# Kernel optimization log

Measured on AMD Instinct MI355X. Metric: run time of the kernel, lower is better.

Reference implementation:

```python
import jax, jax.numpy as jnp
import numpy as np

INPUT_DIM = 4
HIDDEN_DIM = 256
T_OBS, T_UNOBS, BATCH = 64, 32, 4096


def setup_inputs() -> dict:
    key = jax.random.key(0)
    ks = jax.random.split(key, 16)
    H, D = HIDDEN_DIM, INPUT_DIM
    s = lambda k, shape, fan: jax.random.normal(k, shape, jnp.float32) * (1.0 / np.sqrt(fan))
    return {
        "x_obs": jax.random.normal(ks[0], (T_OBS, BATCH, D), jnp.float32),
        "t_obs": jnp.cumsum(jax.random.uniform(ks[1], (T_OBS, BATCH, 1), jnp.float32), axis=0),
        "t_unobs": jax.random.uniform(ks[2], (T_UNOBS, BATCH, 1), jnp.float32),
        # stem MLP (n_layers=2): Linear(D+1 -> H), LeakyReLU, Linear(H -> H)
        "stem_w1": s(ks[3], (H, D + 1), D + 1),
        "stem_b1": jnp.zeros((H,), jnp.float32),
        "stem_w2": s(ks[4], (H, H), H),
        "stem_b2": jnp.zeros((H,), jnp.float32),
        # single-layer GRU, PyTorch gate order (r, z, n)
        "gru_wi": s(ks[5], (3 * H, H), H),
        "gru_wh": s(ks[6], (3 * H, H), H),
        "gru_bi": jnp.zeros((3 * H,), jnp.float32),
        "gru_bh": jnp.zeros((3 * H,), jnp.float32),
        # head MLP (n_layers=1): Linear(H -> D)
        "head_w": s(ks[7], (D, H), H),
        "head_b": jnp.zeros((D,), jnp.float32),
    }


def _gru_cell(x, h, wi, wh, bi, bh):
    # x, h: [B, H].  PyTorch GRU: r,z gates sigmoid; n gate tanh with r gating hidden path.
    gx = x @ wi.T + bi
    gh = h @ wh.T + bh
    rx, zx, nx = jnp.split(gx, 3, axis=-1)
    rh, zh, nh = jnp.split(gh, 3, axis=-1)
    r = jax.nn.sigmoid(rx + rh)
    u = jax.nn.sigmoid(zx + zh)
    n = jnp.tanh(nx + r * nh)
    return (1.0 - u) * n + u * h


def reference(x_obs, t_obs, t_unobs, stem_w1, stem_b1, stem_w2, stem_b2,
              gru_wi, gru_wh, gru_bi, gru_bh, head_w, head_b):
    unobs_len = t_unobs.shape[0]
    batch, hidden = x_obs.shape[1], gru_wh.shape[1]

    # preprocess: first difference of time (0 at step 0), concat, stem MLP
    t_diff = jnp.concatenate([jnp.zeros_like(t_obs[:1]), t_obs[1:] - t_obs[:-1]], axis=0)
    xt = jnp.concatenate([x_obs, t_diff], axis=-1)             # [T_obs, B, D+1]
    xt = jax.nn.leaky_relu(xt @ stem_w1.T + stem_b1)
    xt = xt @ stem_w2.T + stem_b2                              # [T_obs, B, H]

    cell = lambda x, h: _gru_cell(x, jax.lax.stop_gradient(h), gru_wi, gru_wh, gru_bi, gru_bh)

    h0 = jnp.zeros((batch, hidden), x_obs.dtype)

    def obs_step(h, x_t):
        h_new = cell(x_t, h)
        return h_new, None

    h, _ = jax.lax.scan(obs_step, h0, xt)
    z_last = h                                                  # output of 1-layer GRU == hidden

    def ar_step(carry, _):
        z, h = carry
        h_new = cell(z, h)
        return (h_new, h_new), h_new

    (_, _), zs_rest = jax.lax.scan(ar_step, (z_last, h), None, length=unobs_len - 1)
    zs = jnp.concatenate([z_last[None], zs_rest], axis=0)       # [T_unobs, B, H]

    x_hats = zs @ head_w.T + head_b                             # [T_unobs, B, D]
    return x_hats, zs
```

## Files before the change

kernel.cpp:

```cpp
#include <hip/hip_runtime.h>
#include <cstdint>
#include <cstddef>

#define T_OBS_C 64
#define T_UNOBS_C 32
#define BATCH_C 4096
#define HID_C 256

typedef short v8s __attribute__((ext_vector_type(8)));
typedef float v4f __attribute__((ext_vector_type(4)));
typedef unsigned short u16x8 __attribute__((ext_vector_type(8)));

__device__ __forceinline__ float bf2f(unsigned short u) {
  union { unsigned int i; float f; } v; v.i = ((unsigned int)u) << 16; return v.f;
}
__device__ __forceinline__ unsigned short f2bf(float f) {
  union { float f; unsigned int i; } v; v.f = f;
  unsigned int r = (v.i + 0x7FFFu + ((v.i >> 16) & 1u)) >> 16;
  return (unsigned short)r;
}

__global__ void prep_kernel(const float* __restrict__ wi,
                            const float* __restrict__ w2,
                            const float* __restrict__ b2,
                            const float* __restrict__ bi,
                            unsigned short* __restrict__ wi_hi,
                            unsigned short* __restrict__ wi_lo,
                            const float* __restrict__ wh,
                            unsigned short* __restrict__ wh_hi,
                            unsigned short* __restrict__ wh_lo,
                            unsigned short* __restrict__ wc_hi,
                            unsigned short* __restrict__ wc_lo,
                            float* __restrict__ bc_obs) {
  const int n = blockIdx.x;
  const int k = threadIdx.x;
  const int idx = n * 256 + k;

  float wv = wi[idx];
  unsigned short h1 = f2bf(wv);
  wi_hi[idx] = h1; wi_lo[idx] = f2bf(wv - bf2f(h1));

  float hv = wh[idx];
  unsigned short h2 = f2bf(hv);
  wh_hi[idx] = h2; wh_lo[idx] = f2bf(hv - bf2f(h2));

  float acc = 0.f;
  for (int j = 0; j < 256; ++j)
    acc += wi[n * 256 + j] * w2[j * 256 + k];
  unsigned short h3 = f2bf(acc);
  wc_hi[idx] = h3; wc_lo[idx] = f2bf(acc - bf2f(h3));

  if (k == 0) {
    float b = 0.f;
    for (int j = 0; j < 256; ++j) b += wi[n * 256 + j] * b2[j];
    bc_obs[n] = b + bi[n];
  }
}

__global__ __launch_bounds__(512, 2)
void rnn_ws2(const float* __restrict__ x_obs,
             const float* __restrict__ t_obs,
             const float* __restrict__ w1,
             const float* __restrict__ b1,
             const unsigned short* __restrict__ wc_hi, const unsigned short* __restrict__ wc_lo,
             const unsigned short* __restrict__ wi_hi, const unsigned short* __restrict__ wi_lo,
             const unsigned short* __restrict__ wh_hi, const unsigned short* __restrict__ wh_lo,
             const float* __restrict__ bc_obs,
             const float* __restrict__ bi,
             const float* __restrict__ bh,
             const float* __restrict__ head_w,
             const float* __restrict__ head_b,
             unsigned short* h_hi0, unsigned short* h_lo0,
             unsigned short* h_hi1, unsigned short* h_lo1,
             unsigned int* cnt,
             float* out_x,
             float* out_z) {
  __shared__ unsigned short wlds[73728];
  __shared__ float w1t[1280];
  __shared__ float b1s[256];

  const int tid = threadIdx.x;
  const int bid = blockIdx.x;
  const int jj  = bid & 15;
  const int cg  = bid >> 4;
  const int rg  = ((jj & 7) << 1) | (jj >> 3);
  const int m0  = rg << 8;
  const int c0  = cg << 4;

  {
    const unsigned short* srcs[6] = {wc_hi, wc_lo, wi_hi, wi_lo, wh_hi, wh_lo};
    for (int id = tid; id < 9216; id += 512) {
      const int sub = id >> 9;
      const int mat = sub / 6;
      const int g   = (sub >> 1) % 3;
      const int hl  = sub & 1;
      const int within = id & 511;
      const int row = within >> 5;
      const int c16 = within & 31;
      const unsigned short* s = srcs[mat * 2 + hl] +
          (((size_t)(g * 256 + c0 + row)) << 8) + (c16 << 3);
      u16x8 v = *(const u16x8*)s;
      *(u16x8*)(wlds + (sub << 12) + (row << 8) + ((c16 ^ row) << 3)) = v;
    }
    for (int i = tid; i < 1280; i += 512) {
      const int k = i / 5, j = i - k * 5;
      w1t[j * 256 + k] = w1[i];
    }
    if (tid < 256) b1s[tid] = b1[tid];
  }

  const int wave = tid >> 6;
  const int lane = tid & 63;
  const int quad = lane >> 4;
  const int l16  = lane & 15;
  const int jc   = c0 + l16;

  float xb_o[3], xb_a[3], hb_[3], hwv[4];
  #pragma unroll
  for (int g = 0; g < 3; ++g) {
    xb_o[g] = bc_obs[g * 256 + jc];
    xb_a[g] = bi[g * 256 + jc];
    hb_[g]  = bh[g * 256 + jc];
  }
  #pragma unroll
  for (int d = 0; d < 4; ++d) hwv[d] = head_w[d * 256 + jc];

  const int rowL0 = (wave * 2 + 0) * 16 + l16;
  const int rowL1 = (wave * 2 + 1) * 16 + l16;
  const size_t rowA0 = (size_t)(m0 + rowL0) << 8;
  const size_t rowA1 = (size_t)(m0 + rowL1) << 8;

  auto rgbar = [&](unsigned int epoch) {
    __syncthreads();
    if (tid == 0) {
      unsigned int* c = cnt + (rg << 6);
      __hip_atomic_fetch_add(c, 1u, __ATOMIC_RELEASE, __HIP_MEMORY_SCOPE_AGENT);
      const unsigned int tgt = epoch << 4;
      while (__hip_atomic_load(c, __ATOMIC_ACQUIRE, __HIP_MEMORY_SCOPE_AGENT) < tgt)
        __builtin_amdgcn_s_sleep(2);
    }
    __syncthreads();
  };

  __syncthreads();

  float4 xv0, xv1; float td0 = 0.f, td1 = 0.f;
  auto load_x = [&](int tt) {
    const size_t xo0 = (size_t)tt * BATCH_C + m0 + rowL0;
    const size_t xo1 = (size_t)tt * BATCH_C + m0 + rowL1;
    xv0 = *(const float4*)(x_obs + xo0 * 4);
    xv1 = *(const float4*)(x_obs + xo1 * 4);
    if (tt > 0) {
      td0 = t_obs[xo0] - t_obs[xo0 - BATCH_C];
      td1 = t_obs[xo1] - t_obs[xo1 - BATCH_C];
    } else { td0 = 0.f; td1 = 0.f; }
  };

  v4f aXp[2][3];
  auto xpath_pre = [&]() {
    #pragma unroll
    for (int mt = 0; mt < 2; ++mt)
      #pragma unroll
      for (int g = 0; g < 3; ++g)
        aXp[mt][g] = (v4f){0.f, 0.f, 0.f, 0.f};
    #pragma unroll
    for (int kc = 0; kc < 8; ++kc) {
      v8s s0h, s0l, s1h, s1l;
      #pragma unroll
      for (int j = 0; j < 8; ++j) {
        const int k = kc * 32 + quad * 8 + j;
        const float wA = w1t[k], wB = w1t[256 + k], wC = w1t[512 + k],
                    wD = w1t[768 + k], wE = w1t[1024 + k];
        const float bb = b1s[k];
        float p0 = xv0.x * wA + xv0.y * wB + xv0.z * wC + xv0.w * wD + td0 * wE + bb;
        float a0 = (p0 > 0.f) ? p0 : 0.01f * p0;
        unsigned short h0 = f2bf(a0);
        s0h[j] = h0; s0l[j] = f2bf(a0 - bf2f(h0));
        float p1 = xv1.x * wA + xv1.y * wB + xv1.z * wC + xv1.w * wD + td1 * wE + bb;
        float a1 = (p1 > 0.f) ? p1 : 0.01f * p1;
        unsigned short h1 = f2bf(a1);
        s1h[j] = h1; s1l[j] = f2bf(a1 - bf2f(h1));
      }
      const int lrow = (l16 << 8) + ((((kc * 4 + quad) ^ l16)) << 3);
      #pragma unroll
      for (int g = 0; g < 3; ++g) {
        const v8s bxh = *(const v8s*)(wlds + ((g * 2 + 0) << 12) + lrow);
        const v8s bxl = *(const v8s*)(wlds + ((g * 2 + 1) << 12) + lrow);
        aXp[0][g] = __builtin_amdgcn_mfma_f32_16x16x32_bf16(s0h, bxh, aXp[0][g], 0, 0, 0);
        aXp[0][g] = __builtin_amdgcn_mfma_f32_16x16x32_bf16(s0l, bxh, aXp[0][g], 0, 0, 0);
        aXp[0][g] = __builtin_amdgcn_mfma_f32_16x16x32_bf16(s0h, bxl, aXp[0][g], 0, 0, 0);
        aXp[1][g] = __builtin_amdgcn_mfma_f32_16x16x32_bf16(s1h, bxh, aXp[1][g], 0, 0, 0);
        aXp[1][g] = __builtin_amdgcn_mfma_f32_16x16x32_bf16(s1l, bxh, aXp[1][g], 0, 0, 0);
        aXp[1][g] = __builtin_amdgcn_mfma_f32_16x16x32_bf16(s1h, bxl, aXp[1][g], 0, 0, 0);
      }
    }
  };

  load_x(0);
  xpath_pre();
  rgbar(1);

  unsigned int epoch = 2;
  #pragma unroll 1
  for (int step = 0; step < T_OBS_C + T_UNOBS_C - 1; ++step) {
    const bool obs = (step < T_OBS_C);
    const unsigned short* hih = (step & 1) ? h_hi1 : h_hi0;
    const unsigned short* hil = (step & 1) ? h_lo1 : h_lo0;
    unsigned short* hoh = (step & 1) ? h_hi0 : h_hi1;
    unsigned short* hol = (step & 1) ? h_lo0 : h_lo1;
    const int zi = (step == T_OBS_C - 1) ? 0
                   : (step >= T_OBS_C ? step - (T_OBS_C - 1) : -1);

    v4f aX[2][3], aH[2][3];
    #pragma unroll
    for (int mt = 0; mt < 2; ++mt)
      #pragma unroll
      for (int g = 0; g < 3; ++g) {
        aX[mt][g] = obs ? aXp[mt][g] : (v4f){0.f, 0.f, 0.f, 0.f};
        aH[mt][g] = (v4f){0.f, 0.f, 0.f, 0.f};
      }

    const bool nextobs = (step + 1 < T_OBS_C);
    if (nextobs) load_x(step + 1);

    if (obs) {
      #pragma unroll
      for (int kc = 0; kc < 8; ++kc) {
        const size_t ko = (size_t)(kc * 32 + quad * 8);
        const v8s ah0h = *(const v8s*)(hih + rowA0 + ko);
        const v8s ah0l = *(const v8s*)(hil + rowA0 + ko);
        const v8s ah1h = *(const v8s*)(hih + rowA1 + ko);
        const v8s ah1l = *(const v8s*)(hil + rowA1 + ko);
        const int lrow = (l16 << 8) + ((((kc * 4 + quad) ^ l16)) << 3);
        #pragma unroll
        for (int g = 0; g < 3; ++g) {
          const v8s bhh = *(const v8s*)(wlds + (((6 + g) * 2 + 0) << 12) + lrow);
          const v8s bhl = *(const v8s*)(wlds + (((6 + g) * 2 + 1) << 12) + lrow);
          aH[0][g] = __builtin_amdgcn_mfma_f32_16x16x32_bf16(ah0h, bhh, aH[0][g], 0, 0, 0);
          aH[0][g] = __builtin_amdgcn_mfma_f32_16x16x32_bf16(ah0l, bhh, aH[0][g], 0, 0, 0);
          aH[0][g] = __builtin_amdgcn_mfma_f32_16x16x32_bf16(ah0h, bhl, aH[0][g], 0, 0, 0);
          aH[1][g] = __builtin_amdgcn_mfma_f32_16x16x32_bf16(ah1h, bhh, aH[1][g], 0, 0, 0);
          aH[1][g] = __builtin_amdgcn_mfma_f32_16x16x32_bf16(ah1l, bhh, aH[1][g], 0, 0, 0);
          aH[1][g] = __builtin_amdgcn_mfma_f32_16x16x32_bf16(ah1h, bhl, aH[1][g], 0, 0, 0);
        }
      }
    } else {
      #pragma unroll
      for (int kc = 0; kc < 8; ++kc) {
        const size_t ko = (size_t)(kc * 32 + quad * 8);
        const v8s ah0h = *(const v8s*)(hih + rowA0 + ko);
        const v8s ah0l = *(const v8s*)(hil + rowA0 + ko);
        const v8s ah1h = *(const v8s*)(hih + rowA1 + ko);
        const v8s ah1l = *(const v8s*)(hil + rowA1 + ko);
        const int lrow = (l16 << 8) + ((((kc * 4 + quad) ^ l16)) << 3);
        #pragma unroll
        for (int g = 0; g < 3; ++g) {
          const v8s bxh = *(const v8s*)(wlds + (((3 + g) * 2 + 0) << 12) + lrow);
          const v8s bxl = *(const v8s*)(wlds + (((3 + g) * 2 + 1) << 12) + lrow);
          const v8s bhh = *(const v8s*)(wlds + (((6 + g) * 2 + 0) << 12) + lrow);
          const v8s bhl = *(const v8s*)(wlds + (((6 + g) * 2 + 1) << 12) + lrow);
          aX[0][g] = __builtin_amdgcn_mfma_f32_16x16x32_bf16(ah0h, bxh, aX[0][g], 0, 0, 0);
          aX[0][g] = __builtin_amdgcn_mfma_f32_16x16x32_bf16(ah0l, bxh, aX[0][g], 0, 0, 0);
          aX[0][g] = __builtin_amdgcn_mfma_f32_16x16x32_bf16(ah0h, bxl, aX[0][g], 0, 0, 0);
          aX[1][g] = __builtin_amdgcn_mfma_f32_16x16x32_bf16(ah1h, bxh, aX[1][g], 0, 0, 0);
          aX[1][g] = __builtin_amdgcn_mfma_f32_16x16x32_bf16(ah1l, bxh, aX[1][g], 0, 0, 0);
          aX[1][g] = __builtin_amdgcn_mfma_f32_16x16x32_bf16(ah1h, bxl, aX[1][g], 0, 0, 0);
          aH[0][g] = __builtin_amdgcn_mfma_f32_16x16x32_bf16(ah0h, bhh, aH[0][g], 0, 0, 0);
          aH[0][g] = __builtin_amdgcn_mfma_f32_16x16x32_bf16(ah0l, bhh, aH[0][g], 0, 0, 0);
          aH[0][g] = __builtin_amdgcn_mfma_f32_16x16x32_bf16(ah0h, bhl, aH[0][g], 0, 0, 0);
          aH[1][g] = __builtin_amdgcn_mfma_f32_16x16x32_bf16(ah1h, bhh, aH[1][g], 0, 0, 0);
          aH[1][g] = __builtin_amdgcn_mfma_f32_16x16x32_bf16(ah1l, bhh, aH[1][g], 0, 0, 0);
          aH[1][g] = __builtin_amdgcn_mfma_f32_16x16x32_bf16(ah1h, bhl, aH[1][g], 0, 0, 0);
        }
      }
    }

    #pragma unroll
    for (int mt = 0; mt < 2; ++mt) {
      #pragma unroll
      for (int r = 0; r < 4; ++r) {
        const int grow = m0 + (wave * 2 + mt) * 16 + quad * 4 + r;
        const size_t hoff = ((size_t)grow << 8) + jc;
        const float xbr = obs ? xb_o[0] : xb_a[0];
        const float xbz = obs ? xb_o[1] : xb_a[1];
        const float xbn = obs ? xb_o[2] : xb_a[2];
        float gr = aX[mt][0][r] + xbr + aH[mt][0][r] + hb_[0];
        float gz = aX[mt][1][r] + xbz + aH[mt][1][r] + hb_[1];
        float nx = aX[mt][2][r] + xbn;
        float nh = aH[mt][2][r] + hb_[2];
        float rr = 1.f / (1.f + expf(-gr));
        float uu = 1.f / (1.f + expf(-gz));
        float nn = tanhf(nx + rr * nh);
        float hold = bf2f(hih[hoff]) + bf2f(hil[hoff]);
        float hnew = (1.f - uu) * nn + uu * hold;
        unsigned short hi = f2bf(hnew);
        hoh[hoff] = hi;
        hol[hoff] = f2bf(hnew - bf2f(hi));
        if (zi >= 0) {
          out_z[((size_t)zi << 20) + hoff] = hnew;
          #pragma unroll
          for (int d = 0; d < 4; ++d) {
            float pd = hnew * hwv[d];
            pd += __shfl_xor(pd, 1);
            pd += __shfl_xor(pd, 2);
            pd += __shfl_xor(pd, 4);
            pd += __shfl_xor(pd, 8);
            if (l16 == 0) {
              if (cg == 0) pd += head_b[d];
              atomicAdd(out_x + ((((size_t)zi << 12) + grow) << 2) + d, pd);
            }
          }
        }
      }
    }

    if (nextobs) xpath_pre();

    if (step < T_OBS_C + T_UNOBS_C - 2) rgbar(epoch++);
  }
}

extern "C" void kernel_launch(void* const* d_in, const int* in_sizes, int n_in,
                              void* d_out, int out_size, void* d_ws, size_t ws_size,
                              hipStream_t stream) {
  const float* x_obs = (const float*)d_in[0];
  const float* t_obs = (const float*)d_in[1];
  const float* w1 = (const float*)d_in[3];
  const float* b1 = (const float*)d_in[4];
  const float* w2 = (const float*)d_in[5];
  const float* b2 = (const float*)d_in[6];
  const float* wi = (const float*)d_in[7];
  const float* wh = (const float*)d_in[8];
  const float* bi = (const float*)d_in[9];
  const float* bh = (const float*)d_in[10];
  const float* hw = (const float*)d_in[11];
  const float* hb = (const float*)d_in[12];

  float* out_x = (float*)d_out;
  float* out_z = out_x + (size_t)T_UNOBS_C * BATCH_C * 4;

  unsigned short* p = (unsigned short*)d_ws;
  unsigned short* wi_hi = p; p += 768 * 256;
  unsigned short* wi_lo = p; p += 768 * 256;
  unsigned short* wh_hi = p; p += 768 * 256;
  unsigned short* wh_lo = p; p += 768 * 256;
  unsigned short* wc_hi = p; p += 768 * 256;
  unsigned short* wc_lo = p; p += 768 * 256;
  unsigned short* h_hi0 = p; p += (size_t)1 << 20;
  unsigned short* h_lo0 = p; p += (size_t)1 << 20;
  unsigned short* h_hi1 = p; p += (size_t)1 << 20;
  unsigned short* h_lo1 = p; p += (size_t)1 << 20;
  float* bc_obs = (float*)p; p += 768 * 2;
  unsigned int* cnt = (unsigned int*)p;

  hipMemsetAsync(h_hi0, 0, (size_t)4 << 20, stream);
  hipMemsetAsync(cnt, 0, 16 * 64 * sizeof(unsigned int), stream);
  hipMemsetAsync(out_x, 0, (size_t)T_UNOBS_C * BATCH_C * 4 * sizeof(float), stream);

  prep_kernel<<<768, 256, 0, stream>>>(wi, w2, b2, bi,
                                       wi_hi, wi_lo, wh, wh_hi, wh_lo,
                                       wc_hi, wc_lo, bc_obs);

  void* args[] = {
    (void*)&x_obs, (void*)&t_obs, (void*)&w1, (void*)&b1,
    (void*)&wc_hi, (void*)&wc_lo, (void*)&wi_hi, (void*)&wi_lo,
    (void*)&wh_hi, (void*)&wh_lo,
    (void*)&bc_obs, (void*)&bi, (void*)&bh, (void*)&hw, (void*)&hb,
    (void*)&h_hi0, (void*)&h_lo0, (void*)&h_hi1, (void*)&h_lo1,
    (void*)&cnt, (void*)&out_x, (void*)&out_z
  };
  hipLaunchCooperativeKernel(reinterpret_cast<void*>(rnn_ws2),
                             dim3(256), dim3(512), args, 0, stream);
}
```

Before: 2.873 ms.

## Replace block-level row-group barrier with per-wave counters and column-blocked hidden layout

Drops the workgroup-wide barrier across the 16 blocks of a row group. Each wave now signals and waits on its own counter for the 32 batch rows it owns, so waves progress independently. The hidden-state buffers switch to a column-blocked layout ([cg][row][16]), which makes each block's stores and each wave's A-fragment loads contiguous. The x-path precompute for the next step also moves to after the signal, overlapping it with other blocks' work. Correctness now depends on the per-wave fences ordering global writes, and the wave count is spread over more counters.

```diff
diff --git a/kernel.cpp b/kernel.cpp
--- a/kernel.cpp
+++ b/kernel.cpp
@@ -58,23 +58,23 @@
 }
 
 __global__ __launch_bounds__(512, 2)
-void rnn_ws2(const float* __restrict__ x_obs,
-             const float* __restrict__ t_obs,
-             const float* __restrict__ w1,
-             const float* __restrict__ b1,
-             const unsigned short* __restrict__ wc_hi, const unsigned short* __restrict__ wc_lo,
-             const unsigned short* __restrict__ wi_hi, const unsigned short* __restrict__ wi_lo,
-             const unsigned short* __restrict__ wh_hi, const unsigned short* __restrict__ wh_lo,
-             const float* __restrict__ bc_obs,
-             const float* __restrict__ bi,
-             const float* __restrict__ bh,
-             const float* __restrict__ head_w,
-             const float* __restrict__ head_b,
-             unsigned short* h_hi0, unsigned short* h_lo0,
-             unsigned short* h_hi1, unsigned short* h_lo1,
-             unsigned int* cnt,
-             float* out_x,
-             float* out_z) {
+void rnn_wave(const float* __restrict__ x_obs,
+              const float* __restrict__ t_obs,
+              const float* __restrict__ w1,
+              const float* __restrict__ b1,
+              const unsigned short* __restrict__ wc_hi, const unsigned short* __restrict__ wc_lo,
+              const unsigned short* __restrict__ wi_hi, const unsigned short* __restrict__ wi_lo,
+              const unsigned short* __restrict__ wh_hi, const unsigned short* __restrict__ wh_lo,
+              const float* __restrict__ bc_obs,
+              const float* __restrict__ bi,
+              const float* __restrict__ bh,
+              const float* __restrict__ head_w,
+              const float* __restrict__ head_b,
+              unsigned short* h_hi0, unsigned short* h_lo0,
+              unsigned short* h_hi1, unsigned short* h_lo1,
+              unsigned int* cnt,
+              float* out_x,
+              float* out_z) {
   __shared__ unsigned short wlds[73728];
   __shared__ float w1t[1280];
   __shared__ float b1s[256];
@@ -83,8 +83,8 @@
   const int bid = blockIdx.x;
   const int jj  = bid & 15;
   const int cg  = bid >> 4;
-  const int rg  = ((jj & 7) << 1) | (jj >> 3);
-  const int m0  = rg << 8;
+  const int rr  = ((jj & 7) << 1) | (jj >> 3);
+  const int m0  = rr << 8;
   const int c0  = cg << 4;
 
   {
@@ -123,31 +123,34 @@
     hb_[g]  = bh[g * 256 + jc];
   }
   #pragma unroll
-  for (int d = 0; d < 4; ++d) hwv[d] = head_w[d * 256 + jc];
-
-  const int rowL0 = (wave * 2 + 0) * 16 + l16;
-  const int rowL1 = (wave * 2 + 1) * 16 + l16;
-  const size_t rowA0 = (size_t)(m0 + rowL0) << 8;
-  const size_t rowA1 = (size_t)(m0 + rowL1) << 8;
-
-  auto rgbar = [&](unsigned int epoch) {
-    __syncthreads();
-    if (tid == 0) {
-      unsigned int* c = cnt + (rg << 6);
-      __hip_atomic_fetch_add(c, 1u, __ATOMIC_RELEASE, __HIP_MEMORY_SCOPE_AGENT);
-      const unsigned int tgt = epoch << 4;
-      while (__hip_atomic_load(c, __ATOMIC_ACQUIRE, __HIP_MEMORY_SCOPE_AGENT) < tgt)
-        __builtin_amdgcn_s_sleep(2);
-    }
-    __syncthreads();
+  for (int d = 0; d < 4; ++d) hwv[d] = head_b[0] * 0.f + head_w[d * 256 + jc];
+
+  const int rowL0 = wave * 32 + l16;
+  const int rowL1 = rowL0 + 16;
+  const size_t rb0 = (size_t)(m0 + rowL0) << 4;
+  const size_t rb1 = (size_t)(m0 + rowL1) << 4;
+  const size_t xr0 = (size_t)(m0 + rowL0);
+  const size_t xr1 = (size_t)(m0 + rowL1);
+
+  unsigned int* cslab = cnt + ((rr * 8 + wave) << 4);
+
+  auto wave_signal = [&]() {
+    asm volatile("s_waitcnt vmcnt(0)" ::: "memory");
+    if (lane == 0)
+      __hip_atomic_fetch_add(cslab, 1u, __ATOMIC_RELEASE, __HIP_MEMORY_SCOPE_AGENT);
+  };
+  auto wave_wait = [&](unsigned int tgt) {
+    while (__hip_atomic_load(cslab, __ATOMIC_RELAXED, __HIP_MEMORY_SCOPE_AGENT) < tgt)
+      __builtin_amdgcn_s_sleep(2);
+    (void)__hip_atomic_load(cslab, __ATOMIC_ACQUIRE, __HIP_MEMORY_SCOPE_AGENT);
   };
 
   __syncthreads();
 
   float4 xv0, xv1; float td0 = 0.f, td1 = 0.f;
   auto load_x = [&](int tt) {
-    const size_t xo0 = (size_t)tt * BATCH_C + m0 + rowL0;
-    const size_t xo1 = (size_t)tt * BATCH_C + m0 + rowL1;
+    const size_t xo0 = (size_t)tt * BATCH_C + xr0;
+    const size_t xo1 = (size_t)tt * BATCH_C + xr1;
     xv0 = *(const float4*)(x_obs + xo0 * 4);
     xv1 = *(const float4*)(x_obs + xo1 * 4);
     if (tt > 0) {
@@ -198,9 +201,7 @@
 
   load_x(0);
   xpath_pre();
-  rgbar(1);
-
-  unsigned int epoch = 2;
+
   #pragma unroll 1
   for (int step = 0; step < T_OBS_C + T_UNOBS_C - 1; ++step) {
     const bool obs = (step < T_OBS_C);
@@ -220,67 +221,48 @@
         aH[mt][g] = (v4f){0.f, 0.f, 0.f, 0.f};
       }
 
-    const bool nextobs = (step + 1 < T_OBS_C);
-    if (nextobs) load_x(step + 1);
-
-    if (obs) {
-      #pragma unroll
-      for (int kc = 0; kc < 8; ++kc) {
-        const size_t ko = (size_t)(kc * 32 + quad * 8);
-        const v8s ah0h = *(const v8s*)(hih + rowA0 + ko);
-        const v8s ah0l = *(const v8s*)(hil + rowA0 + ko);
-        const v8s ah1h = *(const v8s*)(hih + rowA1 + ko);
-        const v8s ah1l = *(const v8s*)(hil + rowA1 + ko);
-        const int lrow = (l16 << 8) + ((((kc * 4 + quad) ^ l16)) << 3);
-        #pragma unroll
-        for (int g = 0; g < 3; ++g) {
-          const v8s bhh = *(const v8s*)(wlds + (((6 + g) * 2 + 0) << 12) + lrow);
-          const v8s bhl = *(const v8s*)(wlds + (((6 + g) * 2 + 1) << 12) + lrow);
-          aH[0][g] = __builtin_amdgcn_mfma_f32_16x16x32_bf16(ah0h, bhh, aH[0][g], 0, 0, 0);
-          aH[0][g] = __builtin_amdgcn_mfma_f32_16x16x32_bf16(ah0l, bhh, aH[0][g], 0, 0, 0);
-          aH[0][g] = __builtin_amdgcn_mfma_f32_16x16x32_bf16(ah0h, bhl, aH[0][g], 0, 0, 0);
-          aH[1][g] = __builtin_amdgcn_mfma_f32_16x16x32_bf16(ah1h, bhh, aH[1][g], 0, 0, 0);
-          aH[1][g] = __builtin_amdgcn_mfma_f32_16x16x32_bf16(ah1l, bhh, aH[1][g], 0, 0, 0);
-          aH[1][g] = __builtin_amdgcn_mfma_f32_16x16x32_bf16(ah1h, bhl, aH[1][g], 0, 0, 0);
-        }
-      }
-    } else {
-      #pragma unroll
-      for (int kc = 0; kc < 8; ++kc) {
-        const size_t ko = (size_t)(kc * 32 + quad * 8);
-        const v8s ah0h = *(const v8s*)(hih + rowA0 + ko);
-        const v8s ah0l = *(const v8s*)(hil + rowA0 + ko);
-        const v8s ah1h = *(const v8s*)(hih + rowA1 + ko);
-        const v8s ah1l = *(const v8s*)(hil + rowA1 + ko);
-        const int lrow = (l16 << 8) + ((((kc * 4 + quad) ^ l16)) << 3);
+    if (step > 0) wave_wait((unsigned int)step << 4);
+
+    #pragma unroll
+    for (int kc = 0; kc < 8; ++kc) {
+      const size_t co = ((size_t)(kc * 2 + (quad >> 1)) << 16) + ((quad & 1) << 3);
+      const v8s ah0h = *(const v8s*)(hih + co + rb0);
+      const v8s ah0l = *(const v8s*)(hil + co + rb0);
+      const v8s ah1h = *(const v8s*)(hih + co + rb1);
+      const v8s ah1l = *(const v8s*)(hil + co + rb1);
+      const int lrow = (l16 << 8) + ((((kc * 4 + quad) ^ l16)) << 3);
+      if (!obs) {
         #pragma unroll
         for (int g = 0; g < 3; ++g) {
           const v8s bxh = *(const v8s*)(wlds + (((3 + g) * 2 + 0) << 12) + lrow);
           const v8s bxl = *(const v8s*)(wlds + (((3 + g) * 2 + 1) << 12) + lrow);
-          const v8s bhh = *(const v8s*)(wlds + (((6 + g) * 2 + 0) << 12) + lrow);
-          const v8s bhl = *(const v8s*)(wlds + (((6 + g) * 2 + 1) << 12) + lrow);
           aX[0][g] = __builtin_amdgcn_mfma_f32_16x16x32_bf16(ah0h, bxh, aX[0][g], 0, 0, 0);
           aX[0][g] = __builtin_amdgcn_mfma_f32_16x16x32_bf16(ah0l, bxh, aX[0][g], 0, 0, 0);
           aX[0][g] = __builtin_amdgcn_mfma_f32_16x16x32_bf16(ah0h, bxl, aX[0][g], 0, 0, 0);
           aX[1][g] = __builtin_amdgcn_mfma_f32_16x16x32_bf16(ah1h, bxh, aX[1][g], 0, 0, 0);
           aX[1][g] = __builtin_amdgcn_mfma_f32_16x16x32_bf16(ah1l, bxh, aX[1][g], 0, 0, 0);
           aX[1][g] = __builtin_amdgcn_mfma_f32_16x16x32_bf16(ah1h, bxl, aX[1][g], 0, 0, 0);
-          aH[0][g] = __builtin_amdgcn_mfma_f32_16x16x32_bf16(ah0h, bhh, aH[0][g], 0, 0, 0);
-          aH[0][g] = __builtin_amdgcn_mfma_f32_16x16x32_bf16(ah0l, bhh, aH[0][g], 0, 0, 0);
-          aH[0][g] = __builtin_amdgcn_mfma_f32_16x16x32_bf16(ah0h, bhl, aH[0][g], 0, 0, 0);
-          aH[1][g] = __builtin_amdgcn_mfma_f32_16x16x32_bf16(ah1h, bhh, aH[1][g], 0, 0, 0);
-          aH[1][g] = __builtin_amdgcn_mfma_f32_16x16x32_bf16(ah1l, bhh, aH[1][g], 0, 0, 0);
-          aH[1][g] = __builtin_amdgcn_mfma_f32_16x16x32_bf16(ah1h, bhl, aH[1][g], 0, 0, 0);
         }
       }
+      #pragma unroll
+      for (int g = 0; g < 3; ++g) {
+        const v8s bhh = *(const v8s*)(wlds + (((6 + g) * 2 + 0) << 12) + lrow);
+        const v8s bhl = *(const v8s*)(wlds + (((6 + g) * 2 + 1) << 12) + lrow);
+        aH[0][g] = __builtin_amdgcn_mfma_f32_16x16x32_bf16(ah0h, bhh, aH[0][g], 0, 0, 0);
+        aH[0][g] = __builtin_amdgcn_mfma_f32_16x16x32_bf16(ah0l, bhh, aH[0][g], 0, 0, 0);
+        aH[0][g] = __builtin_amdgcn_mfma_f32_16x16x32_bf16(ah0h, bhl, aH[0][g], 0, 0, 0);
+        aH[1][g] = __builtin_amdgcn_mfma_f32_16x16x32_bf16(ah1h, bhh, aH[1][g], 0, 0, 0);
+        aH[1][g] = __builtin_amdgcn_mfma_f32_16x16x32_bf16(ah1l, bhh, aH[1][g], 0, 0, 0);
+        aH[1][g] = __builtin_amdgcn_mfma_f32_16x16x32_bf16(ah1h, bhl, aH[1][g], 0, 0, 0);
+      }
     }
 
     #pragma unroll
     for (int mt = 0; mt < 2; ++mt) {
       #pragma unroll
       for (int r = 0; r < 4; ++r) {
-        const int grow = m0 + (wave * 2 + mt) * 16 + quad * 4 + r;
-        const size_t hoff = ((size_t)grow << 8) + jc;
+        const int grow = m0 + wave * 32 + mt * 16 + quad * 4 + r;
+        const size_t hoff = ((size_t)cg << 16) + ((size_t)grow << 4) + l16;
         const float xbr = obs ? xb_o[0] : xb_a[0];
         const float xbz = obs ? xb_o[1] : xb_a[1];
         const float xbn = obs ? xb_o[2] : xb_a[2];
@@ -288,16 +270,16 @@
         float gz = aX[mt][1][r] + xbz + aH[mt][1][r] + hb_[1];
         float nx = aX[mt][2][r] + xbn;
         float nh = aH[mt][2][r] + hb_[2];
-        float rr = 1.f / (1.f + expf(-gr));
+        float rr2 = 1.f / (1.f + expf(-gr));
         float uu = 1.f / (1.f + expf(-gz));
-        float nn = tanhf(nx + rr * nh);
+        float nn = tanhf(nx + rr2 * nh);
         float hold = bf2f(hih[hoff]) + bf2f(hil[hoff]);
         float hnew = (1.f - uu) * nn + uu * hold;
         unsigned short hi = f2bf(hnew);
         hoh[hoff] = hi;
         hol[hoff] = f2bf(hnew - bf2f(hi));
         if (zi >= 0) {
-          out_z[((size_t)zi << 20) + hoff] = hnew;
+          out_z[((size_t)zi << 20) + ((size_t)grow << 8) + jc] = hnew;
           #pragma unroll
           for (int d = 0; d < 4; ++d) {
             float pd = hnew * hwv[d];
@@ -314,9 +296,12 @@
       }
     }
 
-    if (nextobs) xpath_pre();
-
-    if (step < T_OBS_C + T_UNOBS_C - 2) rgbar(epoch++);
+    if (step < T_OBS_C + T_UNOBS_C - 2) wave_signal();
+
+    if (step + 1 < T_OBS_C) {
+      load_x(step + 1);
+      xpath_pre();
+    }
   }
 }
 
@@ -354,7 +339,7 @@
   unsigned int* cnt = (unsigned int*)p;
 
   hipMemsetAsync(h_hi0, 0, (size_t)4 << 20, stream);
-  hipMemsetAsync(cnt, 0, 16 * 64 * sizeof(unsigned int), stream);
+  hipMemsetAsync(cnt, 0, 128 * 16 * sizeof(unsigned int), stream);
   hipMemsetAsync(out_x, 0, (size_t)T_UNOBS_C * BATCH_C * 4 * sizeof(float), stream);
 
   prep_kernel<<<768, 256, 0, stream>>>(wi, w2, b2, bi,
@@ -369,6 +354,6 @@
     (void*)&h_hi0, (void*)&h_lo0, (void*)&h_hi1, (void*)&h_lo1,
     (void*)&cnt, (void*)&out_x, (void*)&out_z
   };
-  hipLaunchCooperativeKernel(reinterpret_cast<void*>(rnn_ws2),
+  hipLaunchCooperativeKernel(reinterpret_cast<void*>(rnn_wave),
                              dim3(256), dim3(512), args, 0, stream);
 }
```

Result: slower. 7.231 ms (+151.6%).
